# Optimization experiments

Hardware: AMD Instinct MI355X
Metric: run time of the kernel (lower is better)

## Reference

```python
import jax, jax.numpy as jnp
import numpy as np

EPS = 1e-5
POOL_R, POOL_T, SCALE = 5, 7, 0.125  # pool_r, pool_t, 1/pool_stride


def conv_bn_relu(x, W, b, gamma, beta, pad):
    # Conv2d(bias) + BatchNorm2d (training-mode batch stats, biased var) + ReLU
    y = jax.lax.conv_general_dilated(x, W, (1, 1), [(pad, pad), (pad, pad)],
                                     dimension_numbers=('NCHW', 'OIHW', 'NCHW'))
    y = y + b[None, :, None, None]
    mean = y.mean(axis=(0, 2, 3))
    var = y.var(axis=(0, 2, 3))
    y = (y - mean[None, :, None, None]) * jax.lax.rsqrt(var + EPS)[None, :, None, None]
    y = y * gamma[None, :, None, None] + beta[None, :, None, None]
    return jax.nn.relu(y)


def linear_bn_relu(x, W, b, gamma, beta):
    # LinearBlock: Linear + BatchNorm (over batch dim) + ReLU
    y = x @ W.T + b
    mean = y.mean(axis=0)
    var = y.var(axis=0)
    y = (y - mean) * jax.lax.rsqrt(var + EPS) * gamma + beta
    return jax.nn.relu(y)


def _hat_int(x):
    # Antiderivative of the triangular (bilinear) hat kernel at offset x.
    u = jnp.clip(x, -1.0, 1.0)
    return jnp.where(u <= 0, 0.5 * (1.0 + u) ** 2, 0.5 + u - 0.5 * u ** 2)


def prroi_pool(feat, rois, ph, pw, scale):
    # Exact PrRoIPool2D. feat: [B,C,H,W]; rois: [B,N,4] xyxy in image coords.
    # Bilinear interp is a sum of separable hat kernels at integer grid points, so the
    # exact bin integral factorizes into per-axis hat-integral weights Wx, Wy.
    B, C, H, W = feat.shape
    x1, y1, x2, y2 = [rois[..., i] * scale for i in range(4)]
    bw = (x2 - x1) / pw   # [B,N]
    bh = (y2 - y1) / ph
    qx = jnp.arange(pw, dtype=feat.dtype)
    qy = jnp.arange(ph, dtype=feat.dtype)
    xs_lo = x1[..., None] + qx * bw[..., None]   # [B,N,Pw]
    ys_lo = y1[..., None] + qy * bh[..., None]   # [B,N,Ph]
    gw = jnp.arange(W, dtype=feat.dtype)
    gh = jnp.arange(H, dtype=feat.dtype)
    Wx = _hat_int(xs_lo[..., None] + bw[..., None, None] - gw) - _hat_int(xs_lo[..., None] - gw)  # [B,N,Pw,W]
    Wy = _hat_int(ys_lo[..., None] + bh[..., None, None] - gh) - _hat_int(ys_lo[..., None] - gh)  # [B,N,Ph,H]
    out = jnp.einsum('bchw,bnph,bnqw->bncpq', feat, Wy, Wx)
    area = (bw * bh)[:, :, None, None, None]
    return jnp.where(area > 0, out / jnp.maximum(area, 1e-12), 0.0)  # [B,N,C,Ph,Pw]


def _forward(feat1, feat2, bb1, proposals2,
             w_c1r, b_c1r, g_c1r, be_c1r,
             w_c1t, b_c1t, g_c1t, be_c1t,
             w_c2t, b_c2t, g_c2t, be_c2t,
             w_f1r, b_f1r, g_f1r, be_f1r,
             w_f2r, b_f2r, g_f2r, be_f2r,
             w_f1rt, b_f1rt, g_f1rt, be_f1rt,
             w_f2rt, b_f2rt, g_f2rt, be_f2rt,
             w_iou, b_iou):
    S = feat2.shape[0]
    N = proposals2.shape[2]
    # --- get_modulation ---
    c3_r = conv_bn_relu(feat1, w_c1r, b_c1r, g_c1r, be_c1r, 1)
    bb = bb1[0]  # [S,4] xywh -> xyxy
    roi_r = jnp.concatenate([bb[:, :2], bb[:, :2] + bb[:, 2:4]], axis=1)[:, None, :]
    pooled_r = prroi_pool(c3_r, roi_r, POOL_R, POOL_R, SCALE)[:, 0]   # [S,256,5,5]
    m = conv_bn_relu(pooled_r, w_f1r, b_f1r, g_f1r, be_f1r, 0)        # [S,1024,1,1]
    m = conv_bn_relu(m, w_f2r, b_f2r, g_f2r, be_f2r, 0)               # [S,256,1,1]
    modulation = m.reshape(S, -1)                                     # [S,256]
    # --- get_iou_feat ---
    c3_t = conv_bn_relu(conv_bn_relu(feat2, w_c1t, b_c1t, g_c1t, be_c1t, 1),
                        w_c2t, b_c2t, g_c2t, be_c2t, 1)
    # --- predict_iou ---
    c3_t_att = c3_t * modulation[:, :, None, None]
    props = proposals2[0]  # [S,N,4] xywh -> xyxy
    rois_t = jnp.concatenate([props[..., :2], props[..., :2] + props[..., 2:4]], axis=-1)
    pooled_t = prroi_pool(c3_t_att, rois_t, POOL_T, POOL_T, SCALE)    # [S,N,256,7,7]
    x = pooled_t.reshape(S * N, -1)
    x = linear_bn_relu(x, w_f1rt, b_f1rt, g_f1rt, be_f1rt)
    x = linear_bn_relu(x, w_f2rt, b_f2rt, g_f2rt, be_f2rt)
    iou = x @ w_iou.T + b_iou
    return iou.reshape(1, S, N)  # (num_images, num_sequences, num_proposals)


def setup_inputs() -> dict:
    key = jax.random.key(0)
    ks = jax.random.split(key, 8)
    S, C, Hf, Wf, N = 64, 256, 36, 36, 16
    inp = {}
    inp['feat1'] = jax.random.normal(ks[0], (S, C, Hf, Wf), jnp.float32)
    inp['feat2'] = jax.random.normal(ks[1], (S, C, Hf, Wf), jnp.float32)
    xy1 = jax.random.uniform(ks[2], (1, S, 2), minval=20.0, maxval=180.0)
    wh1 = jax.random.uniform(ks[3], (1, S, 2), minval=40.0, maxval=100.0)
    inp['bb1'] = jnp.concatenate([xy1, wh1], axis=-1).astype(jnp.float32)
    xy2 = jax.random.uniform(ks[4], (1, S, N, 2), minval=20.0, maxval=180.0)
    wh2 = jax.random.uniform(ks[5], (1, S, N, 2), minval=40.0, maxval=100.0)
    inp['proposals2'] = jnp.concatenate([xy2, wh2], axis=-1).astype(jnp.float32)

    def kaiming(k, shape):
        fan_in = int(np.prod(shape[1:]))
        return (jax.random.normal(k, shape) * np.sqrt(2.0 / fan_in)).astype(jnp.float32)

    kp = jax.random.split(ks[6], 8)
    specs = [('c1r', (256, C, 3, 3), kp[0]), ('c1t', (256, C, 3, 3), kp[1]),
             ('c2t', (256, 256, 3, 3), kp[2]), ('f1r', (1024, 256, 5, 5), kp[3]),
             ('f2r', (256, 1024, 1, 1), kp[4]), ('f1rt', (1024, 256 * 7 * 7), kp[5]),
             ('f2rt', (1024, 1024), kp[6])]
    for name, shape, k in specs:
        inp['w_' + name] = kaiming(k, shape)
        oc = shape[0]
        inp['b_' + name] = jnp.zeros(oc, jnp.float32)
        inp['g_' + name] = jnp.ones(oc, jnp.float32)
        inp['be_' + name] = jnp.zeros(oc, jnp.float32)
    inp['w_iou'] = kaiming(kp[7], (1, 1024))
    inp['b_iou'] = jnp.zeros(1, jnp.float32)
    return inp


def reference(feat1, feat2, bb1, proposals2,
              w_c1r, b_c1r, g_c1r, be_c1r,
              w_c1t, b_c1t, g_c1t, be_c1t,
              w_c2t, b_c2t, g_c2t, be_c2t,
              w_f1r, b_f1r, g_f1r, be_f1r,
              w_f2r, b_f2r, g_f2r, be_f2r,
              w_f1rt, b_f1rt, g_f1rt, be_f1rt,
              w_f2rt, b_f2rt, g_f2rt, be_f2rt,
              w_iou, b_iou):
    return _forward(feat1, feat2, bb1, proposals2,
                    w_c1r, b_c1r, g_c1r, be_c1r,
                    w_c1t, b_c1t, g_c1t, be_c1t,
                    w_c2t, b_c2t, g_c2t, be_c2t,
                    w_f1r, b_f1r, g_f1r, be_f1r,
                    w_f2r, b_f2r, g_f2r, be_f2r,
                    w_f1rt, b_f1rt, g_f1rt, be_f1rt,
                    w_f2rt, b_f2rt, g_f2rt, be_f2rt,
                    w_iou, b_iou)
```

## Files before the change

kernel.cpp:

```cpp
#include <hip/hip_runtime.h>
#include <cstddef>


typedef _Float16 f16;
typedef __attribute__((ext_vector_type(4))) _Float16 f16x4;
typedef __attribute__((ext_vector_type(8))) _Float16 f16x8;
typedef __attribute__((ext_vector_type(4))) float f32x4;

__device__ __forceinline__ void gload16(const void* g, void* l) {
  __builtin_amdgcn_global_load_lds((const __attribute__((address_space(1))) void*)g,
                                   (__attribute__((address_space(3))) void*)l, 16, 0, 0);
}

#define WAITB(N) asm volatile("s_waitcnt vmcnt(" #N ")\n\ts_barrier" ::: "memory")
#define LGKB()   asm volatile("s_waitcnt lgkmcnt(0)\n\ts_barrier" ::: "memory")

static __device__ __forceinline__ float hat_int(float x) {
  float u = fminf(1.f, fmaxf(-1.f, x));
  float a = 0.5f * (1.f + u) * (1.f + u);
  float b = 0.5f + u - 0.5f * u * u;
  return (u <= 0.f) ? a : b;
}

static __device__ __forceinline__ size_t pk_off(int row, int k, int K) {
  return (size_t)(row >> 7) * ((size_t)K * 128) + (size_t)(k >> 5) * 4096
       + (size_t)((((k >> 3) & 3) * 128 + (row & 127)) * 8 + (k & 7));
}

__global__ void k_zero(float4* __restrict__ p, int n4) {
  int i = blockIdx.x * 256 + threadIdx.x;
  if (i < n4) p[i] = float4{0.f, 0.f, 0.f, 0.f};
}

__global__ void k_border(f16* __restrict__ FT) {
  const int img = blockIdx.x;
  f16* base = FT + (size_t)img * 32 * 1444 * 8;
  for (int i = threadIdx.x; i < 148 * 256; i += 256) {
    int b = i >> 8, c = i & 255;
    int r, cc;
    if (b < 38)       { r = 0;          cc = b; }
    else if (b < 76)  { r = 37;         cc = b - 38; }
    else if (b < 112) { r = b - 76 + 1; cc = 0; }
    else              { r = b - 112 + 1; cc = 37; }
    base[((size_t)(c >> 3) * 1444 + r * 38 + cc) * 8 + (c & 7)] = (f16)0.f;
  }
}

__global__ void k_pad(const float* __restrict__ src, f16* __restrict__ FT) {
  const int img = blockIdx.x, h = blockIdx.y, c = threadIdx.x;
  const float* sp = src + ((size_t)img * 256 + c) * 1296 + h * 36;
  f16* op = FT + (((size_t)img * 32 + (c >> 3)) * 1444 + (h + 1) * 38 + 1) * 8 + (c & 7);
#pragma unroll 4
  for (int w = 0; w < 36; ++w) op[w * 8] = (f16)sp[w];
}

__global__ void k_pad2(const f16* __restrict__ yH, f16* __restrict__ FT,
                       const float* __restrict__ mean, const float* __restrict__ istd,
                       const float* __restrict__ g, const float* __restrict__ be) {
  const int img = blockIdx.x, h = blockIdx.y, c = threadIdx.x;
  const float sc = istd[c] * g[c];
  const float sh = be[c] - mean[c] * sc;
  const f16* sp = yH + ((size_t)img * 1296 + h * 36) * 256 + c;
  f16* op = FT + (((size_t)img * 32 + (c >> 3)) * 1444 + (h + 1) * 38 + 1) * 8 + (c & 7);
#pragma unroll 4
  for (int w = 0; w < 36; ++w) {
    float v = fmaxf(fmaf((float)sp[w * 256], sc, sh), 0.f);
    op[w * 8] = (f16)v;
  }
}

__global__ void k_pack_wc(const float* __restrict__ w, f16* __restrict__ dst) {
  int i = blockIdx.x * 256 + threadIdx.x;
  int oct = i / 294912;
  int r = i - oct * 294912;
  int ks = r >> 12;
  int r2 = r & 4095;
  int koct = r2 >> 10;
  int r3 = r2 & 1023;
  int row = r3 >> 3, kj = r3 & 7;
  int k = ks * 32 + koct * 8 + kj;
  int t = k >> 8, c = k & 255;
  int oc = oct * 128 + row;
  dst[i] = (f16)w[(oc * 256 + c) * 9 + t];
}

__global__ __launch_bounds__(256) void k_packx_h(
    const f16* __restrict__ src, f16* __restrict__ dst, int M, int K) {
  __shared__ f16 sT[128][264];
  const int k0 = blockIdx.x * 256, r0 = blockIdx.y * 128;
  const int t = threadIdx.x;
  const int rl = t >> 5, kk = (t & 31) * 8;
  for (int rnd = 0; rnd < 16; ++rnd) {
    const int row_l = rl + rnd * 8;
    const int row = r0 + row_l;
    if (row < M) {
      f16x8 v = *reinterpret_cast<const f16x8*>(src + (size_t)row * K + k0 + kk);
      *reinterpret_cast<f16x8*>(&sT[row_l][kk]) = v;
    }
  }
  __syncthreads();
  const size_t base = (size_t)(r0 >> 7) * ((size_t)K * 128) + (size_t)(k0 >> 5) * 4096;
#pragma unroll
  for (int cs = 0; cs < 8; ++cs) {
#pragma unroll
    for (int half = 0; half < 2; ++half) {
      const int e = half * 256 + t;
      const int koct = e >> 7, row_l = e & 127;
      if (r0 + row_l < M) {
        f16x8 v = *reinterpret_cast<const f16x8*>(&sT[row_l][cs * 32 + koct * 8]);
        *reinterpret_cast<f16x8*>(dst + base + (size_t)cs * 4096 + e * 8) = v;
      }
    }
  }
}

__global__ __launch_bounds__(256) void k_packx_f(
    const float* __restrict__ src, f16* __restrict__ dst, int M, int K) {
  __shared__ f16 sT[128][264];
  const int k0 = blockIdx.x * 256, r0 = blockIdx.y * 128;
  const int t = threadIdx.x;
  const int rl = t >> 5, kk = (t & 31) * 8;
  for (int rnd = 0; rnd < 16; ++rnd) {
    const int row_l = rl + rnd * 8;
    const int row = r0 + row_l;
    if (row < M) {
      const float4* sp = reinterpret_cast<const float4*>(src + (size_t)row * K + k0 + kk);
      float4 a = sp[0], b = sp[1];
      f16* o = &sT[row_l][kk];
      o[0] = (f16)a.x; o[1] = (f16)a.y; o[2] = (f16)a.z; o[3] = (f16)a.w;
      o[4] = (f16)b.x; o[5] = (f16)b.y; o[6] = (f16)b.z; o[7] = (f16)b.w;
    }
  }
  __syncthreads();
  const size_t base = (size_t)(r0 >> 7) * ((size_t)K * 128) + (size_t)(k0 >> 5) * 4096;
#pragma unroll
  for (int cs = 0; cs < 8; ++cs) {
#pragma unroll
    for (int half = 0; half < 2; ++half) {
      const int e = half * 256 + t;
      const int koct = e >> 7, row_l = e & 127;
      if (r0 + row_l < M) {
        f16x8 v = *reinterpret_cast<const f16x8*>(&sT[row_l][cs * 32 + koct * 8]);
        *reinterpret_cast<f16x8*>(dst + base + (size_t)cs * 4096 + e * 8) = v;
      }
    }
  }
}

__global__ __launch_bounds__(256) void k_conv_mfma(
    const f16* __restrict__ Wpk, const f16* __restrict__ FT2,
    const float* __restrict__ bias, f16* __restrict__ yH) {
  __shared__ f16x8 sA[1536];
  __shared__ f16x8 sB[1536];
  const int bid = blockIdx.x;
  const int orig = (bid & 7) * 176 + (bid >> 3);
  const int img = orig / 22;
  const int rem = orig - img * 22;
  const int oct = rem / 11;
  const int pt  = rem - oct * 11;
  const int m0 = oct * 128;
  const int p0 = pt * 128;
  const int tid = threadIdx.x;
  const int lane = tid & 63;
  const int wv = tid >> 6;
  const int wr = wv >> 1, wc = wv & 1;

  const f16* aBase = Wpk + (size_t)oct * 294912 + wv * 1024 + lane * 8;
  const f16* ftImg = FT2 + (size_t)img * 32 * 1444 * 8;
  int pos0 = p0 + lane;
  int pc0 = min(pos0, 1295);
  int pc1 = min(pos0 + 64, 1295);
  int pb0 = (pc0 / 36) * 38 + (pc0 % 36);
  int pb1 = (pc1 / 36) * 38 + (pc1 % 36);

  const int loff = wv * 2048 + lane * 16;

  auto stage = [&](int buf, int ks) {
    const int t = ks >> 3;
    const int dy = t / 3, dx = t - dy * 3;
    const int cs = ks & 7;
    const int dyx = dy * 38 + dx;
    char* lA = (char*)sA + buf * 8192 + loff;
    char* lB = (char*)sB + buf * 8192 + loff;
    const f16* ap = aBase + (size_t)ks * 4096;
    const f16* bp = ftImg + ((size_t)(cs * 4 + wv) * 1444 + dyx) * 8;
    gload16(ap, lA);
    gload16(ap + 512, lA + 1024);
    gload16(bp + pb0 * 8, lB);
    gload16(bp + pb1 * 8, lB + 1024);
  };

  f32x4 acc[4][4] = {};
  const int fidxA = ((lane >> 4) << 7) + wr * 64 + (lane & 15);
  const int fidxB = ((lane >> 4) << 7) + wc * 64 + (lane & 15);

  stage(0, 0); stage(1, 1); stage(2, 2);
  int cur = 0;
  for (int ks = 0; ks < 72; ++ks) {
    const int r = 71 - ks;
    if (r >= 2)      WAITB(8);
    else if (r == 1) WAITB(4);
    else             WAITB(0);
    const int base = cur * 512;
    f16x8 af[4], bf[4];
#pragma unroll
    for (int i = 0; i < 4; ++i) {
      af[i] = sA[base + fidxA + i * 16];
      bf[i] = sB[base + fidxB + i * 16];
    }
#pragma unroll
    for (int i = 0; i < 4; ++i)
#pragma unroll
      for (int j = 0; j < 4; ++j)
        acc[i][j] = __builtin_amdgcn_mfma_f32_16x16x32_f16(af[i], bf[j], acc[i][j], 0, 0, 0);
    LGKB();
    if (ks + 3 < 72) stage(cur, ks + 3);
    cur = (cur == 2) ? 0 : cur + 1;
  }

  const int colb = p0 + wc * 64 + (lane & 15);
  const int rowb = m0 + wr * 64 + ((lane >> 4) << 2);
  f16* yb = yH + (size_t)img * 1296 * 256;
#pragma unroll
  for (int i = 0; i < 4; ++i) {
    const int oc0 = rowb + i * 16;
    float b0 = bias[oc0], b1 = bias[oc0 + 1], b2 = bias[oc0 + 2], b3 = bias[oc0 + 3];
#pragma unroll
    for (int j = 0; j < 4; ++j) {
      const int col = colb + j * 16;
      if (col < 1296) {
        f16x4 v;
        v[0] = (f16)(acc[i][j][0] + b0);
        v[1] = (f16)(acc[i][j][1] + b1);
        v[2] = (f16)(acc[i][j][2] + b2);
        v[3] = (f16)(acc[i][j][3] + b3);
        *reinterpret_cast<f16x4*>(yb + (size_t)col * 256 + oc0) = v;
      }
    }
  }
}

__global__ __launch_bounds__(256) void k_gemm_f16pk(
    const f16* __restrict__ Apk, const f16* __restrict__ Bpk,
    float* __restrict__ part, int K, int Nout, int stepsPerZ, int mrows) {
  __shared__ f16x8 sA[1536];
  __shared__ f16x8 sB[1536];
  const int nt = blockIdx.x, mt = blockIdx.y, z = blockIdx.z;
  const int tid = threadIdx.x;
  const int lane = tid & 63;
  const int wv = tid >> 6;
  const int wr = wv >> 1, wc = wv & 1;

  const f16* aC = Apk + (size_t)mt * K * 128 + wv * 1024 + lane * 8;
  const f16* bC = Bpk + (size_t)nt * K * 128 + wv * 1024 + lane * 8;
  const int loff = wv * 2048 + lane * 16;

  auto stage = [&](int buf, int ks) {
    char* lA = (char*)sA + buf * 8192 + loff;
    char* lB = (char*)sB + buf * 8192 + loff;
    const f16* ap = aC + (size_t)ks * 4096;
    const f16* bp = bC + (size_t)ks * 4096;
    gload16(ap, lA);
    gload16(ap + 512, lA + 1024);
    gload16(bp, lB);
    gload16(bp + 512, lB + 1024);
  };

  f32x4 acc[4][4] = {};
  const int fidxA = ((lane >> 4) << 7) + wr * 64 + (lane & 15);
  const int fidxB = ((lane >> 4) << 7) + wc * 64 + (lane & 15);

  const int ks0 = z * stepsPerZ;
  stage(0, ks0); stage(1, ks0 + 1); stage(2, ks0 + 2);
  int cur = 0;
  for (int i = 0; i < stepsPerZ; ++i) {
    const int r = stepsPerZ - 1 - i;
    if (r >= 2)      WAITB(8);
    else if (r == 1) WAITB(4);
    else             WAITB(0);
    const int base = cur * 512;
    f16x8 af[4], bf[4];
#pragma unroll
    for (int j = 0; j < 4; ++j) {
      af[j] = sA[base + fidxA + j * 16];
      bf[j] = sB[base + fidxB + j * 16];
    }
#pragma unroll
    for (int ii = 0; ii < 4; ++ii)
#pragma unroll
      for (int jj = 0; jj < 4; ++jj)
        acc[ii][jj] = __builtin_amdgcn_mfma_f32_16x16x32_f16(af[ii], bf[jj], acc[ii][jj], 0, 0, 0);
    LGKB();
    if (i + 3 < stepsPerZ) stage(cur, ks0 + i + 3);
    cur = (cur == 2) ? 0 : cur + 1;
  }

  const size_t zoff = (size_t)z * mrows * Nout;
  const int colb = nt * 128 + wc * 64 + (lane & 15);
  const int rowb = mt * 128 + wr * 64 + ((lane >> 4) << 2);
#pragma unroll
  for (int i = 0; i < 4; ++i)
#pragma unroll
    for (int j = 0; j < 4; ++j)
#pragma unroll
      for (int r = 0; r < 4; ++r)
        part[zoff + (size_t)(rowb + i * 16 + r) * Nout + colb + j * 16] = acc[i][j][r];
}

__global__ void k_reduce(const float* __restrict__ part, const float* __restrict__ bias,
                         float* __restrict__ out, int mrows, int Mout, int Nout, int sk) {
  int i = blockIdx.x * 256 + threadIdx.x;
  if (i >= Mout * Nout) return;
  int row = i / Nout, col = i - row * Nout;
  float s = bias[col];
  for (int z = 0; z < sk; ++z)
    s += part[(size_t)z * mrows * Nout + (size_t)row * Nout + col];
  out[i] = s;
}

__global__ void k_chan_stats_hwc(const f16* __restrict__ yH,
                                 float* __restrict__ psum, float* __restrict__ psq) {
  const int z = blockIdx.x, c = threadIdx.x;
  const f16* p = yH + (size_t)z * 256 * 256 + c;
  float s = 0.f, ss = 0.f;
#pragma unroll 4
  for (int i = 0; i < 256; ++i) {
    float v = (float)p[(size_t)i * 256];
    s += v; ss += v * v;
  }
  psum[z * 256 + c] = s;
  psq[z * 256 + c] = ss;
}

__global__ void k_chan_stats_hwc_final(const float* __restrict__ psum,
                                       const float* __restrict__ psq,
                                       float* __restrict__ mean, float* __restrict__ istd) {
  const int c = threadIdx.x;
  float s = 0.f, ss = 0.f;
  for (int z = 0; z < 324; ++z) { s += psum[z * 256 + c]; ss += psq[z * 256 + c]; }
  float m = s * (1.f / 82944.f);
  float var = ss * (1.f / 82944.f) - m * m;
  mean[c] = m;
  istd[c] = rsqrtf(var + 1e-5f);
}

__global__ void k_wxy(const float* __restrict__ rois, int ntot, int P,
                      float* __restrict__ Wx, float* __restrict__ Wy,
                      float* __restrict__ area,
                      int* __restrict__ HLO, int* __restrict__ HCNT,
                      int* __restrict__ WLO) {
  int idx = blockIdx.x * blockDim.x + threadIdx.x;
  if (idx >= ntot) return;
  float rx = rois[idx * 4 + 0], ry = rois[idx * 4 + 1];
  float rw = rois[idx * 4 + 2], rh = rois[idx * 4 + 3];
  float x1 = rx * 0.125f, y1 = ry * 0.125f;
  float x2 = (rx + rw) * 0.125f, y2 = (ry + rh) * 0.125f;
  float bw = (x2 - x1) / P, bh = (y2 - y1) / P;
  area[idx] = bw * bh;
  int hlo = max(0, (int)ceilf(y1 - 1.f));
  int hhi = min(35, (int)floorf(y2 + 1.f));
  HLO[idx] = hlo;
  HCNT[idx] = max(0, hhi - hlo + 1);
  for (int q = 0; q < P; ++q) {
    float xlo = x1 + q * bw, ylo = y1 + q * bh;
    WLO[idx * P + q] = min(31, max(0, (int)ceilf(xlo - 1.f)));
    for (int g = 0; g < 36; ++g) {
      float fg = (float)g;
      Wx[(idx * P + q) * 36 + g] = hat_int(xlo + bw - fg) - hat_int(xlo - fg);
      Wy[(idx * P + q) * 36 + g] = hat_int(ylo + bh - fg) - hat_int(ylo - fg);
    }
  }
}

template <int P, bool MOD>
__global__ __launch_bounds__(256) void k_pool(
    const f16* __restrict__ feat, const float* __restrict__ Wx,
    const float* __restrict__ Wy, const float* __restrict__ area,
    const int* __restrict__ HLO, const int* __restrict__ HCNT,
    const int* __restrict__ WLO,
    const float* __restrict__ mean, const float* __restrict__ istd,
    const float* __restrict__ g, const float* __restrict__ be,
    const float* __restrict__ mod, f16* __restrict__ out, int N) {
  const int s = blockIdx.x, n = blockIdx.y;
  const int idx = s * N + n;
  const int c = threadIdx.x;
  constexpr int KD = P * P * 256;
  __shared__ f16 sOut[KD];
  __shared__ float sWx[P * 36], sWy[P * 36];
  __shared__ int sWLO[P];
  __shared__ int sH[2];
  for (int i = threadIdx.x; i < P * 36; i += 256) {
    sWx[i] = Wx[(size_t)idx * P * 36 + i];
    sWy[i] = Wy[(size_t)idx * P * 36 + i];
  }
  if (threadIdx.x < P) sWLO[threadIdx.x] = WLO[idx * P + threadIdx.x];
  if (threadIdx.x == 0) { sH[0] = HLO[idx]; sH[1] = HCNT[idx]; }
  __syncthreads();
  const float sc = istd[c] * g[c];
  const float sh = be[c] - mean[c] * sc;
  const f16* f = feat + (size_t)s * 1296 * 256 + c;
  float o[P][P] = {};
  const int hlo = sH[0], hcnt = sH[1];
  for (int hh = 0; hh < hcnt; ++hh) {
    const int h = hlo + hh;
    const f16* rp = f + (size_t)h * 36 * 256;
    float colsum[P];
#pragma unroll
    for (int q = 0; q < P; ++q) {
      const int w0 = sWLO[q];
      const f16* wp = rp + (size_t)w0 * 256;
      float v = 0.f;
#pragma unroll
      for (int j = 0; j < 5; ++j) {
        float x = fmaxf(fmaf((float)wp[j * 256], sc, sh), 0.f);
        v = fmaf(sWx[q * 36 + w0 + j], x, v);
      }
      colsum[q] = v;
    }
#pragma unroll
    for (int p = 0; p < P; ++p) {
      const float wy = sWy[p * 36 + h];
      if (wy != 0.f) {
#pragma unroll
        for (int q = 0; q < P; ++q) o[p][q] = fmaf(wy, colsum[q], o[p][q]);
      }
    }
  }
  float a = area[idx];
  float inv = (a > 0.f) ? 1.f / fmaxf(a, 1e-12f) : 0.f;
  float msc = MOD ? (mod[s * 256 + c] * inv) : inv;
  const int kbase = c * (P * P);
#pragma unroll
  for (int p = 0; p < P; ++p)
#pragma unroll
    for (int q = 0; q < P; ++q)
      sOut[kbase + p * P + q] = (f16)(o[p][q] * msc);
  __syncthreads();
  f16* op = out + (size_t)idx * KD;
  for (int j = threadIdx.x; j < KD; j += 256) op[j] = sOut[j];
}

__global__ void k_fc_stats_part(const float* __restrict__ y, int M, int Nf, int rpz,
                                float* __restrict__ psum, float* __restrict__ psq) {
  int col = blockIdx.x * 256 + threadIdx.x;
  int z = blockIdx.y;
  if (col >= Nf) return;
  int r0 = z * rpz;
  int r1 = min(M, r0 + rpz);
  float s = 0.f, ss = 0.f;
  for (int m = r0; m < r1; ++m) {
    float v = y[(size_t)m * Nf + col];
    s += v; ss += v * v;
  }
  psum[(size_t)z * Nf + col] = s;
  psq[(size_t)z * Nf + col] = ss;
}

__global__ void k_fc_stats_final(const float* __restrict__ psum, const float* __restrict__ psq,
                                 int nz, int Nf, int M,
                                 float* __restrict__ mean, float* __restrict__ istd) {
  int col = blockIdx.x * 256 + threadIdx.x;
  if (col >= Nf) return;
  float s = 0.f, ss = 0.f;
  for (int z = 0; z < nz; ++z) {
    s += psum[(size_t)z * Nf + col];
    ss += psq[(size_t)z * Nf + col];
  }
  float mu = s / (float)M;
  float var = ss / (float)M - mu * mu;
  mean[col] = mu;
  istd[col] = rsqrtf(var + 1e-5f);
}

__global__ void k_fc_bn_relu(float* __restrict__ y, const float* __restrict__ mean,
                             const float* __restrict__ istd, const float* __restrict__ g,
                             const float* __restrict__ be, int total, int Nf) {
  int i = blockIdx.x * 256 + threadIdx.x;
  if (i >= total) return;
  int col = i % Nf;
  float sc = istd[col] * g[col];
  float sh = be[col] - mean[col] * sc;
  y[i] = fmaxf(fmaf(y[i], sc, sh), 0.f);
}

__global__ void k_fc_bn_relu_pk(const float* __restrict__ y, const float* __restrict__ mean,
                                const float* __restrict__ istd, const float* __restrict__ g,
                                const float* __restrict__ be, f16* __restrict__ xpk,
                                int total, int Nf) {
  int i = blockIdx.x * 256 + threadIdx.x;
  if (i >= total) return;
  int row = i / Nf, col = i - row * Nf;
  float sc = istd[col] * g[col];
  float sh = be[col] - mean[col] * sc;
  float v = fmaxf(fmaf(y[i], sc, sh), 0.f);
  xpk[pk_off(row, col, Nf)] = (f16)v;
}

__global__ void k_iou(const float* __restrict__ x, const float* __restrict__ w,
                      const float* __restrict__ b, float* __restrict__ out) {
  const int r = blockIdx.x, tid = threadIdx.x;
  float s = 0.f;
  for (int k = tid; k < 1024; k += 256) s = fmaf(x[(size_t)r * 1024 + k], w[k], s);
  __shared__ float red[256];
  red[tid] = s;
  __syncthreads();
  for (int o = 128; o > 0; o >>= 1) {
    if (tid < o) red[tid] += red[tid + o];
    __syncthreads();
  }
  if (tid == 0) out[r] = red[0] + b[0];
}

static const size_t O_A      = 0;
static const size_t O_POOLT  = 12000000;
static const size_t O_PSUM   = 13000000;
static const size_t O_PSQ    = 13065536;
static const size_t O_WPK2RT = 16000000;
static const size_t O_POOLR  = 18500000;
static const size_t O_WPK2R  = 20000000;
static const size_t O_FT     = 21233664;
static const size_t O_X2PK   = 21233664 + 6422528;
static const size_t O_WC     = 33062912;
static const size_t O_WPK1RT = 33357824;
static const size_t O_WPK1R  = 39780352;
static const size_t O_PRPK   = 43057152;
static const size_t O_Y1     = 43466752;
static const size_t O_Y2     = 44515328;
static const size_t O_MOD    = 45563904;
static const size_t O_WXR    = 45580288;
static const size_t O_WYR    = 45591808;
static const size_t O_ARR    = 45603328;
static const size_t O_WXT    = 45603392;
static const size_t O_WYT    = 45861440;
static const size_t O_ART    = 46119488;
static const size_t O_MEAN   = 46120512;
static const size_t O_ISTD   = 46121536;
static const size_t O_X1PK   = 46122560;
static const size_t O_META   = 46188096;
static const size_t O_PSC    = 46197760;

extern "C" void kernel_launch(void* const* d_in, const int* in_sizes, int n_in,
                              void* d_out, int out_size, void* d_ws, size_t ws_size,
                              hipStream_t stream) {
  (void)in_sizes; (void)n_in; (void)out_size; (void)ws_size;
  const float* feat1  = (const float*)d_in[0];
  const float* feat2  = (const float*)d_in[1];
  const float* bb1    = (const float*)d_in[2];
  const float* props  = (const float*)d_in[3];
  const float* w_c1r  = (const float*)d_in[4];
  const float* b_c1r  = (const float*)d_in[5];
  const float* g_c1r  = (const float*)d_in[6];
  const float* be_c1r = (const float*)d_in[7];
  const float* w_c1t  = (const float*)d_in[8];
  const float* b_c1t  = (const float*)d_in[9];
  const float* g_c1t  = (const float*)d_in[10];
  const float* be_c1t = (const float*)d_in[11];
  const float* w_c2t  = (const float*)d_in[12];
  const float* b_c2t  = (const float*)d_in[13];
  const float* g_c2t  = (const float*)d_in[14];
  const float* be_c2t = (const float*)d_in[15];
  const float* w_f1r  = (const float*)d_in[16];
  const float* b_f1r  = (const float*)d_in[17];
  const float* g_f1r  = (const float*)d_in[18];
  const float* be_f1r = (const float*)d_in[19];
  const float* w_f2r  = (const float*)d_in[20];
  const float* b_f2r  = (const float*)d_in[21];
  const float* g_f2r  = (const float*)d_in[22];
  const float* be_f2r = (const float*)d_in[23];
  const float* w_f1rt = (const float*)d_in[24];
  const float* b_f1rt = (const float*)d_in[25];
  const float* g_f1rt = (const float*)d_in[26];
  const float* be_f1rt= (const float*)d_in[27];
  const float* w_f2rt = (const float*)d_in[28];
  const float* b_f2rt = (const float*)d_in[29];
  const float* g_f2rt = (const float*)d_in[30];
  const float* be_f2rt= (const float*)d_in[31];
  const float* w_iou  = (const float*)d_in[32];
  const float* b_iou  = (const float*)d_in[33];

  float* ws    = (float*)d_ws;
  f16*   AH    = (f16*)(ws + O_A);
  float* PART  = ws + O_A;
  f16*   POOLT = (f16*)(ws + O_POOLT);
  float* PSUM  = ws + O_PSUM;
  float* PSQ   = ws + O_PSQ;
  f16*   WPK2RT= (f16*)(ws + O_WPK2RT);
  f16*   POOLR = (f16*)(ws + O_POOLR);
  f16*   WPK2R = (f16*)(ws + O_WPK2R);
  f16*   FT2   = (f16*)(ws + O_FT);
  f16*   PHPK  = FT2;
  f16*   X2PK  = (f16*)(ws + O_X2PK);
  f16*   WC    = (f16*)(ws + O_WC);
  f16*   WPK1RT= (f16*)(ws + O_WPK1RT);
  f16*   WPK1R = (f16*)(ws + O_WPK1R);
  f16*   PRPK  = (f16*)(ws + O_PRPK);
  float* Y1    = ws + O_Y1;
  float* Y2    = ws + O_Y2;
  float* MODp  = ws + O_MOD;
  float* WXR   = ws + O_WXR;
  float* WYR   = ws + O_WYR;
  float* ARR   = ws + O_ARR;
  float* WXT   = ws + O_WXT;
  float* WYT   = ws + O_WYT;
  float* ART   = ws + O_ART;
  float* MEAN  = ws + O_MEAN;
  float* ISTD  = ws + O_ISTD;
  f16*   X1PK  = (f16*)(ws + O_X1PK);
  int*   META  = (int*)(ws + O_META);
  float* PSUMC = ws + O_PSC;
  float* PSQC  = ws + O_PSC + 82944;
  int* HLOR = META;
  int* HCNTR= META + 64;
  int* WLOR = META + 128;
  int* HLOT = META + 448;
  int* HCNTT= META + 1472;
  int* WLOT = META + 2496;

  k_border<<<64, 256, 0, stream>>>(FT2);
  k_pack_wc<<<2304, 256, 0, stream>>>(w_c1r, WC);
  k_pad<<<dim3(64, 36), 256, 0, stream>>>(feat1, FT2);
  k_conv_mfma<<<1408, 256, 0, stream>>>(WC, FT2, b_c1r, AH);
  k_chan_stats_hwc<<<324, 256, 0, stream>>>(AH, PSUMC, PSQC);
  k_chan_stats_hwc_final<<<1, 256, 0, stream>>>(PSUMC, PSQC, MEAN, ISTD);

  k_wxy<<<1, 64, 0, stream>>>(bb1, 64, 5, WXR, WYR, ARR, HLOR, HCNTR, WLOR);
  k_zero<<<400, 256, 0, stream>>>((float4*)PRPK, 102400);
  k_pool<5, false><<<dim3(64, 1), 256, 0, stream>>>(
      AH, WXR, WYR, ARR, HLOR, HCNTR, WLOR, MEAN, ISTD, g_c1r, be_c1r, nullptr, POOLR, 1);
  k_packx_h<<<dim3(25, 1), 256, 0, stream>>>(POOLR, PRPK, 64, 6400);

  k_packx_f<<<dim3(25, 8), 256, 0, stream>>>(w_f1r, WPK1R, 1024, 6400);
  k_gemm_f16pk<<<dim3(8, 1, 8), 256, 0, stream>>>(PRPK, WPK1R, PART, 6400, 1024, 25, 128);
  k_reduce<<<256, 256, 0, stream>>>(PART, b_f1r, Y1, 128, 64, 1024, 8);
  k_fc_stats_part<<<dim3(4, 8), 256, 0, stream>>>(Y1, 64, 1024, 8, PSUM, PSQ);
  k_fc_stats_final<<<4, 256, 0, stream>>>(PSUM, PSQ, 8, 1024, 64, MEAN, ISTD);
  k_zero<<<64, 256, 0, stream>>>((float4*)X1PK, 16384);
  k_fc_bn_relu_pk<<<256, 256, 0, stream>>>(Y1, MEAN, ISTD, g_f1r, be_f1r, X1PK, 64 * 1024, 1024);

  k_packx_f<<<dim3(4, 2), 256, 0, stream>>>(w_f2r, WPK2R, 256, 1024);
  k_gemm_f16pk<<<dim3(2, 1, 4), 256, 0, stream>>>(X1PK, WPK2R, PART, 1024, 256, 8, 128);
  k_reduce<<<64, 256, 0, stream>>>(PART, b_f2r, MODp, 128, 64, 256, 4);
  k_fc_stats_part<<<dim3(1, 8), 256, 0, stream>>>(MODp, 64, 256, 8, PSUM, PSQ);
  k_fc_stats_final<<<1, 256, 0, stream>>>(PSUM, PSQ, 8, 256, 64, MEAN, ISTD);
  k_fc_bn_relu<<<64, 256, 0, stream>>>(MODp, MEAN, ISTD, g_f2r, be_f2r, 64 * 256, 256);

  k_pack_wc<<<2304, 256, 0, stream>>>(w_c1t, WC);
  k_pad<<<dim3(64, 36), 256, 0, stream>>>(feat2, FT2);
  k_conv_mfma<<<1408, 256, 0, stream>>>(WC, FT2, b_c1t, AH);
  k_chan_stats_hwc<<<324, 256, 0, stream>>>(AH, PSUMC, PSQC);
  k_chan_stats_hwc_final<<<1, 256, 0, stream>>>(PSUMC, PSQC, MEAN, ISTD);
  k_pad2<<<dim3(64, 36), 256, 0, stream>>>(AH, FT2, MEAN, ISTD, g_c1t, be_c1t);

  k_pack_wc<<<2304, 256, 0, stream>>>(w_c2t, WC);
  k_conv_mfma<<<1408, 256, 0, stream>>>(WC, FT2, b_c2t, AH);
  k_chan_stats_hwc<<<324, 256, 0, stream>>>(AH, PSUMC, PSQC);
  k_chan_stats_hwc_final<<<1, 256, 0, stream>>>(PSUMC, PSQC, MEAN, ISTD);

  k_wxy<<<16, 64, 0, stream>>>(props, 1024, 7, WXT, WYT, ART, HLOT, HCNTT, WLOT);
  k_pool<7, true><<<dim3(64, 16), 256, 0, stream>>>(
      AH, WXT, WYT, ART, HLOT, HCNTT, WLOT, MEAN, ISTD, g_c2t, be_c2t, MODp, POOLT, 16);
  k_packx_h<<<dim3(49, 8), 256, 0, stream>>>(POOLT, PHPK, 1024, 12544);

  k_packx_f<<<dim3(49, 8), 256, 0, stream>>>(w_f1rt, WPK1RT, 1024, 12544);
  k_gemm_f16pk<<<dim3(8, 8, 8), 256, 0, stream>>>(PHPK, WPK1RT, PART, 12544, 1024, 49, 1024);
  k_reduce<<<4096, 256, 0, stream>>>(PART, b_f1rt, Y1, 1024, 1024, 1024, 8);
  k_fc_stats_part<<<dim3(4, 64), 256, 0, stream>>>(Y1, 1024, 1024, 16, PSUM, PSQ);
  k_fc_stats_final<<<4, 256, 0, stream>>>(PSUM, PSQ, 64, 1024, 1024, MEAN, ISTD);
  k_fc_bn_relu_pk<<<4096, 256, 0, stream>>>(Y1, MEAN, ISTD, g_f1rt, be_f1rt, X2PK, 1024 * 1024, 1024);

  k_packx_f<<<dim3(4, 8), 256, 0, stream>>>(w_f2rt, WPK2RT, 1024, 1024);
  k_gemm_f16pk<<<dim3(8, 8, 4), 256, 0, stream>>>(X2PK, WPK2RT, PART, 1024, 1024, 8, 1024);
  k_reduce<<<4096, 256, 0, stream>>>(PART, b_f2rt, Y2, 1024, 1024, 1024, 4);
  k_fc_stats_part<<<dim3(4, 64), 256, 0, stream>>>(Y2, 1024, 1024, 16, PSUM, PSQ);
  k_fc_stats_final<<<4, 256, 0, stream>>>(PSUM, PSQ, 64, 1024, 1024, MEAN, ISTD);
  k_fc_bn_relu<<<4096, 256, 0, stream>>>(Y2, MEAN, ISTD, g_f2rt, be_f2rt, 1024 * 1024, 1024);

  k_iou<<<1024, 256, 0, stream>>>(Y2, w_iou, b_iou, (float*)d_out);
}
```

Before: 951.0 us.

## Load A fragments directly from global into registers, stage only B in LDS

In both the conv and GEMM MFMA kernels, the A operand (weights) is no longer staged through LDS. Each lane now reads its MFMA fragments straight from global memory into registers, double-buffered across two register sets. B stays in LDS, with the pipeline cut from triple to double buffering. This removes half the LDS traffic and footprint, at the cost of more registers, shallower prefetch depth, and wait counts that now mix register-destined and LDS-destined loads.

Measured after the change: 1.0000 ms. 5.2% more time.

```diff
diff --git a/kernel.cpp b/kernel.cpp
--- a/kernel.cpp
+++ b/kernel.cpp
@@ -14,6 +14,12 @@
 
 #define WAITB(N) asm volatile("s_waitcnt vmcnt(" #N ")\n\ts_barrier" ::: "memory")
 #define LGKB()   asm volatile("s_waitcnt lgkmcnt(0)\n\ts_barrier" ::: "memory")
+
+#define LOADA(DST, BASE, KS)                                                   \
+  {                                                                            \
+    _Pragma("unroll") for (int _i = 0; _i < 4; ++_i)                           \
+      DST[_i] = *reinterpret_cast<const f16x8*>((BASE) + (size_t)(KS) * 4096 + _i * 128); \
+  }
 
 static __device__ __forceinline__ float hat_int(float x) {
   float u = fminf(1.f, fmaxf(-1.f, x));
@@ -150,8 +156,7 @@
 __global__ __launch_bounds__(256) void k_conv_mfma(
     const f16* __restrict__ Wpk, const f16* __restrict__ FT2,
     const float* __restrict__ bias, f16* __restrict__ yH) {
-  __shared__ f16x8 sA[1536];
-  __shared__ f16x8 sB[1536];
+  __shared__ f16x8 sB[1024];
   const int bid = blockIdx.x;
   const int orig = (bid & 7) * 176 + (bid >> 3);
   const int img = orig / 22;
@@ -165,7 +170,8 @@
   const int wv = tid >> 6;
   const int wr = wv >> 1, wc = wv & 1;
 
-  const f16* aBase = Wpk + (size_t)oct * 294912 + wv * 1024 + lane * 8;
+  const f16* aFrag = Wpk + (size_t)oct * 294912 + ((lane >> 4) << 10)
+                   + ((size_t)(wr * 64 + (lane & 15)) << 3);
   const f16* ftImg = FT2 + (size_t)img * 32 * 1444 * 8;
   int pos0 = p0 + lane;
   int pc0 = min(pos0, 1295);
@@ -175,48 +181,42 @@
 
   const int loff = wv * 2048 + lane * 16;
 
-  auto stage = [&](int buf, int ks) {
+  auto stageB = [&](int buf, int ks) {
     const int t = ks >> 3;
     const int dy = t / 3, dx = t - dy * 3;
     const int cs = ks & 7;
     const int dyx = dy * 38 + dx;
-    char* lA = (char*)sA + buf * 8192 + loff;
     char* lB = (char*)sB + buf * 8192 + loff;
-    const f16* ap = aBase + (size_t)ks * 4096;
     const f16* bp = ftImg + ((size_t)(cs * 4 + wv) * 1444 + dyx) * 8;
-    gload16(ap, lA);
-    gload16(ap + 512, lA + 1024);
     gload16(bp + pb0 * 8, lB);
     gload16(bp + pb1 * 8, lB + 1024);
   };
 
   f32x4 acc[4][4] = {};
-  const int fidxA = ((lane >> 4) << 7) + wr * 64 + (lane & 15);
   const int fidxB = ((lane >> 4) << 7) + wc * 64 + (lane & 15);
-
-  stage(0, 0); stage(1, 1); stage(2, 2);
-  int cur = 0;
-  for (int ks = 0; ks < 72; ++ks) {
-    const int r = 71 - ks;
-    if (r >= 2)      WAITB(8);
-    else if (r == 1) WAITB(4);
-    else             WAITB(0);
-    const int base = cur * 512;
-    f16x8 af[4], bf[4];
-#pragma unroll
-    for (int i = 0; i < 4; ++i) {
-      af[i] = sA[base + fidxA + i * 16];
-      bf[i] = sB[base + fidxB + i * 16];
-    }
-#pragma unroll
-    for (int i = 0; i < 4; ++i)
-#pragma unroll
-      for (int j = 0; j < 4; ++j)
-        acc[i][j] = __builtin_amdgcn_mfma_f32_16x16x32_f16(af[i], bf[j], acc[i][j], 0, 0, 0);
-    LGKB();
-    if (ks + 3 < 72) stage(cur, ks + 3);
-    cur = (cur == 2) ? 0 : cur + 1;
-  }
+  f16x8 afA[4], afB[4];
+
+  stageB(0, 0); LOADA(afA, aFrag, 0);
+  stageB(1, 1); LOADA(afB, aFrag, 1);
+
+#define CONV_STEP(AF, BUF, KS)                                                 \
+  {                                                                            \
+    if ((KS) < 71) WAITB(6); else WAITB(0);                                    \
+    f16x8 bf[4];                                                               \
+    _Pragma("unroll") for (int j = 0; j < 4; ++j)                              \
+      bf[j] = sB[(BUF) * 512 + fidxB + j * 16];                                \
+    _Pragma("unroll") for (int ii = 0; ii < 4; ++ii)                           \
+      _Pragma("unroll") for (int jj = 0; jj < 4; ++jj)                         \
+        acc[ii][jj] = __builtin_amdgcn_mfma_f32_16x16x32_f16(AF[ii], bf[jj], acc[ii][jj], 0, 0, 0); \
+    LGKB();                                                                    \
+    if ((KS) + 2 < 72) { stageB(BUF, (KS) + 2); LOADA(AF, aFrag, (KS) + 2); }  \
+  }
+
+  for (int ks = 0; ks < 72; ks += 2) {
+    CONV_STEP(afA, 0, ks);
+    CONV_STEP(afB, 1, ks + 1);
+  }
+#undef CONV_STEP
 
   const int colb = p0 + wc * 64 + (lane & 15);
   const int rowb = m0 + wr * 64 + ((lane >> 4) << 2);
@@ -243,57 +243,55 @@
 __global__ __launch_bounds__(256) void k_gemm_f16pk(
     const f16* __restrict__ Apk, const f16* __restrict__ Bpk,
     float* __restrict__ part, int K, int Nout, int stepsPerZ, int mrows) {
-  __shared__ f16x8 sA[1536];
-  __shared__ f16x8 sB[1536];
+  __shared__ f16x8 sB[1024];
   const int nt = blockIdx.x, mt = blockIdx.y, z = blockIdx.z;
   const int tid = threadIdx.x;
   const int lane = tid & 63;
   const int wv = tid >> 6;
   const int wr = wv >> 1, wc = wv & 1;
 
-  const f16* aC = Apk + (size_t)mt * K * 128 + wv * 1024 + lane * 8;
+  const f16* aFrag = Apk + (size_t)mt * K * 128 + ((lane >> 4) << 10)
+                   + ((size_t)(wr * 64 + (lane & 15)) << 3);
   const f16* bC = Bpk + (size_t)nt * K * 128 + wv * 1024 + lane * 8;
   const int loff = wv * 2048 + lane * 16;
 
-  auto stage = [&](int buf, int ks) {
-    char* lA = (char*)sA + buf * 8192 + loff;
+  auto stageB = [&](int buf, int ks) {
     char* lB = (char*)sB + buf * 8192 + loff;
-    const f16* ap = aC + (size_t)ks * 4096;
     const f16* bp = bC + (size_t)ks * 4096;
-    gload16(ap, lA);
-    gload16(ap + 512, lA + 1024);
     gload16(bp, lB);
     gload16(bp + 512, lB + 1024);
   };
 
   f32x4 acc[4][4] = {};
-  const int fidxA = ((lane >> 4) << 7) + wr * 64 + (lane & 15);
   const int fidxB = ((lane >> 4) << 7) + wc * 64 + (lane & 15);
+  f16x8 afA[4], afB[4];
 
   const int ks0 = z * stepsPerZ;
-  stage(0, ks0); stage(1, ks0 + 1); stage(2, ks0 + 2);
-  int cur = 0;
-  for (int i = 0; i < stepsPerZ; ++i) {
-    const int r = stepsPerZ - 1 - i;
-    if (r >= 2)      WAITB(8);
-    else if (r == 1) WAITB(4);
-    else             WAITB(0);
-    const int base = cur * 512;
-    f16x8 af[4], bf[4];
-#pragma unroll
-    for (int j = 0; j < 4; ++j) {
-      af[j] = sA[base + fidxA + j * 16];
-      bf[j] = sB[base + fidxB + j * 16];
-    }
-#pragma unroll
-    for (int ii = 0; ii < 4; ++ii)
-#pragma unroll
-      for (int jj = 0; jj < 4; ++jj)
-        acc[ii][jj] = __builtin_amdgcn_mfma_f32_16x16x32_f16(af[ii], bf[jj], acc[ii][jj], 0, 0, 0);
-    LGKB();
-    if (i + 3 < stepsPerZ) stage(cur, ks0 + i + 3);
-    cur = (cur == 2) ? 0 : cur + 1;
-  }
+  stageB(0, ks0); LOADA(afA, aFrag, ks0);
+  stageB(1, ks0 + 1); LOADA(afB, aFrag, ks0 + 1);
+
+#define GEMM_STEP(AF, BUF, I)                                                  \
+  {                                                                            \
+    if ((I) + 1 < stepsPerZ) WAITB(6); else WAITB(0);                          \
+    f16x8 bf[4];                                                               \
+    _Pragma("unroll") for (int j = 0; j < 4; ++j)                              \
+      bf[j] = sB[(BUF) * 512 + fidxB + j * 16];                                \
+    _Pragma("unroll") for (int ii = 0; ii < 4; ++ii)                           \
+      _Pragma("unroll") for (int jj = 0; jj < 4; ++jj)                         \
+        acc[ii][jj] = __builtin_amdgcn_mfma_f32_16x16x32_f16(AF[ii], bf[jj], acc[ii][jj], 0, 0, 0); \
+    LGKB();                                                                    \
+    if ((I) + 2 < stepsPerZ) { stageB(BUF, ks0 + (I) + 2); LOADA(AF, aFrag, ks0 + (I) + 2); } \
+  }
+
+  int i2 = 0;
+  for (; i2 + 1 < stepsPerZ; i2 += 2) {
+    GEMM_STEP(afA, 0, i2);
+    GEMM_STEP(afB, 1, i2 + 1);
+  }
+  if (i2 < stepsPerZ) {
+    GEMM_STEP(afA, 0, i2);
+  }
+#undef GEMM_STEP
 
   const size_t zoff = (size_t)z * mrows * Nout;
   const int colb = nt * 128 + wc * 64 + (lane & 15);
```
